# Performance work log

Hardware: AMD Instinct MI355X
Metric: run time of the kernel (lower is better)

The kernel has to match this reference:

```python
import jax, jax.numpy as jnp
import numpy as np

B, XDIM, S = 32768, 32, 16
N_COMBINE = XDIM - 2  # 30 combines with out_channels=S (block0 + middle blocks)


def setup_inputs() -> dict:
    key = jax.random.key(0)
    k1, k2, k3, k4 = jax.random.split(key, 4)
    x = jax.random.randint(k1, (B, XDIM), 0, 2, dtype=jnp.int32)  # binary data
    leaf_logits = jax.random.normal(k2, (XDIM, S), dtype=jnp.float32)  # Bernoulli leaf logits per var
    sum_weights = jax.random.normal(k3, (N_COMBINE, S * S, S), dtype=jnp.float32)
    sum_weights_last = jax.random.normal(k4, (S * S, 1), dtype=jnp.float32)
    return {"x": x, "leaf_logits": leaf_logits, "sum_weights": sum_weights,
            "sum_weights_last": sum_weights_last}


def _combine(a, b, W):
    # a, b: [B, S] log-likelihoods; W: [S*S, OC] raw sum weights.
    # CrossProduct in log domain: out[:, i*S + j] = a[:, i] + b[:, j]
    cross = (a[:, :, None] + b[:, None, :]).reshape(a.shape[0], S * S)  # [B, S*S]
    logw = jax.nn.log_softmax(W, axis=0)  # normalize over in_channels
    # Sum node in log domain: logsumexp over input channels
    return jax.nn.logsumexp(cross[:, :, None] + logw[None, :, :], axis=1)  # [B, OC]


def reference(x, leaf_logits, sum_weights, sum_weights_last):
    xf = x.astype(jnp.float32)[:, :, None]  # [B, XDIM, 1]
    # Bernoulli leaf log-prob: x*log(sigmoid(l)) + (1-x)*log(1-sigmoid(l))
    lp = (xf * jax.nn.log_sigmoid(leaf_logits)[None]
          + (1.0 - xf) * jax.nn.log_sigmoid(-leaf_logits)[None])  # [B, XDIM, S]

    # block 0: combine leaves of vars 0 and 1
    curr = _combine(lp[:, 0], lp[:, 1], sum_weights[0])  # [B, S]

    # middle blocks: fold in vars 2 .. XDIM-2
    mid_leaves = jnp.swapaxes(lp[:, 2:XDIM - 1], 0, 1)  # [XDIM-3, B, S]

    def step(c, inp):
        leaf, W = inp
        return _combine(c, leaf, W), None

    curr, _ = jax.lax.scan(step, curr, (mid_leaves, sum_weights[1:]))

    # final block: fold in last var with out_channels=1 root sum
    out = _combine(curr, lp[:, XDIM - 1], sum_weights_last)  # [B, 1]
    return out[:, None, :]  # [B, 1, 1] to match torch output shape
```

## Files before the change

kernel.cpp:

```cpp
#include <hip/hip_runtime.h>

using uint = unsigned int;

#define DW_LO    0
#define DW_HIb   7616
#define DW_FT    15232
#define DW_DELTA 15360
#define DW_BASE  15392
#define DW_EB0   15396
#define DW_TOT   15616

template<int K>
__device__ __forceinline__ int roti(int x) {
    return __builtin_amdgcn_update_dpp(0, x, 0x120 | K, 0xF, 0xF, true);
}
template<int K>
__device__ __forceinline__ float rotf(float x) {
    return __builtin_bit_cast(float, roti<K>(__builtin_bit_cast(int, x)));
}
__device__ __forceinline__ float logsig(float z) {
    return fminf(z, 0.f) - log1pf(__expf(-fabsf(z)));
}
__device__ __forceinline__ uint bfpack(float a, float b) {
    uint ua = __builtin_bit_cast(uint, a);
    uint ub = __builtin_bit_cast(uint, b);
    ua = (ua + 0x7fffu + ((ua >> 16) & 1u)) >> 16;
    ub = ((ub + 0x7fffu + ((ub >> 16) & 1u)) >> 16) << 16;
    return ua | ub;
}
__device__ __forceinline__ float blo(uint u) { return __builtin_bit_cast(float, u << 16); }
__device__ __forceinline__ float bhi(uint u) { return __builtin_bit_cast(float, u & 0xffff0000u); }

__global__ __launch_bounds__(1024) void prep(const float* __restrict__ sw,
                                             const float* __restrict__ swl,
                                             const float* __restrict__ ll,
                                             float* __restrict__ ws) {
    __shared__ __align__(16) float SW[16384];
    __shared__ float EB[128];
    __shared__ float CM[64], CS[64];
    __shared__ float WF[2048];
    __shared__ float T12[2048];
    __shared__ float MM[4096];
    __shared__ float WL[32];
    __shared__ float BMs[64];

    const int tid = threadIdx.x;
    const int t = blockIdx.x;
    const int lid = tid & 15;

    int s1 = roti<1>(lid) & 15,   s2 = roti<2>(lid) & 15,   s3 = roti<3>(lid) & 15;
    int s4 = roti<4>(lid) & 15,   s5 = roti<5>(lid) & 15,   s6 = roti<6>(lid) & 15;
    int s7 = roti<7>(lid) & 15,   s8 = roti<8>(lid) & 15,   s9 = roti<9>(lid) & 15;
    int s10 = roti<10>(lid) & 15, s11 = roti<11>(lid) & 15, s12 = roti<12>(lid) & 15;
    int s13 = roti<13>(lid) & 15, s14 = roti<14>(lid) & 15, s15 = roti<15>(lid) & 15;

    if (t < 7) {
        const float4* src = (const float4*)sw + t * 4096;
        #pragma unroll
        for (int k = 0; k < 4; ++k) ((float4*)SW)[tid + 1024 * k] = src[tid + 1024 * k];
        if (tid < 128) {
            int cc = tid >> 5, bb = (tid >> 4) & 1, var = 4 * t + 1 + cc;
            float l = ll[var * 16 + lid];
            float lp = bb ? logsig(l) : logsig(-l);
            float m = lp;
            m = fmaxf(m, rotf<1>(m)); m = fmaxf(m, rotf<2>(m));
            m = fmaxf(m, rotf<4>(m)); m = fmaxf(m, rotf<8>(m));
            EB[tid] = __expf(lp - m);
        }
        __syncthreads();
        {
            int grp = tid >> 4, cc = grp >> 4, ocx = grp & 15;
            float m = -1e30f;
            #pragma unroll
            for (int i = 0; i < 16; ++i)
                m = fmaxf(m, SW[cc * 4096 + i * 256 + lid * 16 + ocx]);
            m = fmaxf(m, rotf<1>(m)); m = fmaxf(m, rotf<2>(m));
            m = fmaxf(m, rotf<4>(m)); m = fmaxf(m, rotf<8>(m));
            if (lid == 0) CM[grp] = m;
        }
        __syncthreads();
        {
            int base = tid * 16;
            const float* cmp = CM + ((base >> 12) << 4);
            #pragma unroll
            for (int e = 0; e < 16; ++e) SW[base + e] = __expf(SW[base + e] - cmp[e]);
        }
        __syncthreads();
        {
            int grp = tid >> 4, cc = grp >> 4, ocx = grp & 15;
            float s = 0.f;
            #pragma unroll
            for (int i = 0; i < 16; ++i) s += SW[cc * 4096 + i * 256 + lid * 16 + ocx];
            s += rotf<1>(s); s += rotf<2>(s); s += rotf<4>(s); s += rotf<8>(s);
            if (lid == 0) CS[grp] = 1.0f / s;
        }
        __syncthreads();
        #pragma unroll
        for (int q = 0; q < 2; ++q) {
            int e = tid + q * 1024;
            int cb = e >> 8, cc = cb >> 1, i = (e >> 4) & 15, ocx = e & 15;
            float a = 0.f;
            #pragma unroll
            for (int j = 0; j < 16; ++j)
                a += EB[cb * 16 + j] * SW[cc * 4096 + i * 256 + j * 16 + ocx];
            WF[e] = a * CS[cc * 16 + ocx];
        }
        __syncthreads();
        {
            int bb = tid >> 8, i = (tid >> 4) & 15, l = lid;
            float a = 0.f, a2 = 0.f;
            #pragma unroll
            for (int k = 0; k < 16; ++k) {
                a  += WF[(bb & 1) * 256 + i * 16 + k]       * WF[(2 + (bb >> 1)) * 256 + k * 16 + l];
                a2 += WF[(4 + (bb & 1)) * 256 + i * 16 + k] * WF[(6 + (bb >> 1)) * 256 + k * 16 + l];
            }
            T12[tid] = a;
            T12[1024 + tid] = a2;
        }
        __syncthreads();
        #pragma unroll
        for (int q = 0; q < 4; ++q) {
            int e = tid + q * 1024;
            int v = e >> 8, i = (e >> 4) & 15, ocx = e & 15;
            float a = 0.f;
            #pragma unroll
            for (int k = 0; k < 16; ++k)
                a += T12[(v & 3) * 256 + i * 16 + k] * T12[1024 + (v >> 2) * 256 + k * 16 + ocx];
            MM[e] = a;
        }
        __syncthreads();
        if (tid < 256) {
            int v = tid >> 4, ocx = lid;
            const float* m = MM + v * 256;
            float x0 = m[ocx * 16 + ocx];
            float x1 = m[s1 * 16 + ocx],   x2 = m[s2 * 16 + ocx],   x3 = m[s3 * 16 + ocx];
            float x4 = m[s4 * 16 + ocx],   x5 = m[s5 * 16 + ocx],   x6 = m[s6 * 16 + ocx];
            float x7 = m[s7 * 16 + ocx],   x8 = m[s8 * 16 + ocx],   x9 = m[s9 * 16 + ocx];
            float x10 = m[s10 * 16 + ocx], x11 = m[s11 * 16 + ocx], x12 = m[s12 * 16 + ocx];
            float x13 = m[s13 * 16 + ocx], x14 = m[s14 * 16 + ocx], x15 = m[s15 * 16 + ocx];
            uint4 lo4, hi4;
            lo4.x = bfpack(x0, x1);   lo4.y = bfpack(x2, x3);
            lo4.z = bfpack(x4, x5);   lo4.w = bfpack(x6, x7);
            hi4.x = bfpack(x8, x9);   hi4.y = bfpack(x10, x11);
            hi4.z = bfpack(x12, x13); hi4.w = bfpack(x14, x15);
            uint* wsu = (uint*)ws;
            int dw = t * 1088 + v * 68 + ocx * 4;
            *(uint4*)(wsu + dw) = lo4;
            *(uint4*)(wsu + DW_HIb + dw) = hi4;
        }
    } else {
        const float4* s28 = (const float4*)(sw + 28 * 4096);
        #pragma unroll
        for (int k = 0; k < 2; ++k) ((float4*)SW)[tid + 1024 * k] = s28[tid + 1024 * k];
        if (tid < 64) ((float4*)SW)[2048 + tid] = ((const float4*)swl)[tid];
        if (tid < 96) {
            int cb = tid >> 4, bb = cb & 1;
            int var = (cb < 4) ? (29 + (cb >> 1)) : 31;
            float l = ll[var * 16 + lid];
            float lp = bb ? logsig(l) : logsig(-l);
            float m = lp;
            m = fmaxf(m, rotf<1>(m)); m = fmaxf(m, rotf<2>(m));
            m = fmaxf(m, rotf<4>(m)); m = fmaxf(m, rotf<8>(m));
            EB[tid] = __expf(lp - m);
        }
        __syncthreads();
        if (tid < 528) {
            int grp = tid >> 4;
            float m = -1e30f;
            if (grp < 32) {
                int cc = grp >> 4, ocx = grp & 15;
                #pragma unroll
                for (int i = 0; i < 16; ++i)
                    m = fmaxf(m, SW[cc * 4096 + i * 256 + lid * 16 + ocx]);
            } else {
                #pragma unroll
                for (int i = 0; i < 16; ++i)
                    m = fmaxf(m, SW[8192 + i * 16 + lid]);
            }
            m = fmaxf(m, rotf<1>(m)); m = fmaxf(m, rotf<2>(m));
            m = fmaxf(m, rotf<4>(m)); m = fmaxf(m, rotf<8>(m));
            if (lid == 0) CM[grp] = m;
        }
        __syncthreads();
        for (int idx = tid; idx < 8448; idx += 1024) {
            float cm = (idx < 8192) ? CM[((idx >> 12) << 4) | (idx & 15)] : CM[32];
            SW[idx] = __expf(SW[idx] - cm);
        }
        __syncthreads();
        if (tid < 528) {
            int grp = tid >> 4;
            float s = 0.f;
            if (grp < 32) {
                int cc = grp >> 4, ocx = grp & 15;
                #pragma unroll
                for (int i = 0; i < 16; ++i) s += SW[cc * 4096 + i * 256 + lid * 16 + ocx];
            } else {
                #pragma unroll
                for (int i = 0; i < 16; ++i) s += SW[8192 + i * 16 + lid];
            }
            s += rotf<1>(s); s += rotf<2>(s); s += rotf<4>(s); s += rotf<8>(s);
            if (lid == 0) CS[grp] = 1.0f / s;
        }
        __syncthreads();
        {
            int cb = tid >> 8, cc = cb >> 1, i = (tid >> 4) & 15, ocx = lid;
            float a = 0.f;
            #pragma unroll
            for (int j = 0; j < 16; ++j)
                a += EB[cb * 16 + j] * SW[cc * 4096 + i * 256 + j * 16 + ocx];
            WF[tid] = a * CS[cc * 16 + ocx];
        }
        if (tid < 32) {
            int bb = tid >> 4;
            float a = 0.f;
            #pragma unroll
            for (int j = 0; j < 16; ++j)
                a += EB[(4 + bb) * 16 + j] * SW[8192 + lid * 16 + j];
            WL[tid] = a * CS[32];
        }
        __syncthreads();
        {
            int b01 = tid >> 8, i = (tid >> 4) & 15, l = lid;
            float a = 0.f;
            #pragma unroll
            for (int k = 0; k < 16; ++k)
                a += WF[(b01 & 1) * 256 + i * 16 + k] * WF[(2 + (b01 >> 1)) * 256 + k * 16 + l];
            T12[tid] = a;
        }
        __syncthreads();
        if (tid < 128) {
            int v = tid >> 4;
            float a = 0.f;
            #pragma unroll
            for (int l = 0; l < 16; ++l)
                a += T12[(v & 3) * 256 + lid * 16 + l] * WL[(v >> 2) * 16 + l];
            ws[DW_FT + v * 16 + lid] = a;
        }
        if (tid >= 128 && tid < 192) {
            int u = tid - 128, var = u >> 1, bb = u & 1;
            float m = -1e30f;
            #pragma unroll
            for (int j = 0; j < 16; ++j) {
                float l = ll[var * 16 + j];
                m = fmaxf(m, bb ? logsig(l) : logsig(-l));
            }
            BMs[u] = m;
        }
        if (tid >= 192 && tid < 224) {
            int u = tid - 192, bb = u >> 4, j = u & 15;
            float m = -1e30f;
            #pragma unroll
            for (int jj = 0; jj < 16; ++jj) {
                float l = ll[jj];
                m = fmaxf(m, bb ? logsig(l) : logsig(-l));
            }
            float l = ll[j];
            ws[DW_EB0 + u] = __expf((bb ? logsig(l) : logsig(-l)) - m);
        }
        __syncthreads();
        if (tid < 32) ws[DW_DELTA + tid] = BMs[2 * tid + 1] - BMs[2 * tid];
        if (tid >= 64 && tid < 128) {
            int u = tid - 64;
            float vb = (u < 32) ? BMs[2 * u] : 0.f;
            #pragma unroll
            for (int off = 32; off >= 1; off >>= 1) vb += __shfl_xor(vb, off);
            if (u == 0) ws[DW_BASE] = vb;
        }
    }
}

__global__ __launch_bounds__(512, 4) void spn_main(const int* __restrict__ x,
                                                   const float* __restrict__ ws,
                                                   float* __restrict__ out) {
    __shared__ __align__(16) float sL[DW_TOT];
    const int tid = threadIdx.x;
    const int g = tid >> 4, oc = tid & 15;
    const int b = blockIdx.x * 32 + g;

    int2 xv = *(const int2*)(x + b * 32 + 2 * oc);
    unsigned long long m0 = __ballot(xv.x & 1);
    unsigned long long m1 = __ballot(xv.y & 1);
    const int gw = g & 3;
    unsigned be = (unsigned)(m0 >> (gw * 16)) & 0xffffu;
    unsigned bo = (unsigned)(m1 >> (gw * 16)) & 0xffffu;
    unsigned bits = 0;
    #pragma unroll
    for (int k = 0; k < 16; ++k)
        bits |= (((be >> k) & 1u) << (2 * k)) | (((bo >> k) & 1u) << (2 * k + 1));

    for (int k = tid; k < DW_TOT / 4; k += 512)
        ((float4*)sL)[k] = ((const float4*)ws)[k];
    __syncthreads();

    float2 dl = *(const float2*)(sL + DW_DELTA + 2 * oc);
    float part = 0.f;
    if (xv.x & 1) part += dl.x;
    if (xv.y & 1) part += dl.y;
    part += rotf<1>(part); part += rotf<2>(part);
    part += rotf<4>(part); part += rotf<8>(part);
    float L = sL[DW_BASE] + part;

    float acc = sL[DW_EB0 + (bits & 1) * 16 + oc];
    const uint* sPT = (const uint*)sL;
    const int ocd = oc * 4;

    #pragma unroll
    for (int p = 0; p < 7; ++p) {
        int v = (bits >> (4 * p + 1)) & 15;
        int dw = p * 1088 + v * 68 + ocd;
        uint4 wl4 = *(const uint4*)(sPT + dw);
        uint4 wh4 = *(const uint4*)(sPT + DW_HIb + dw);

        float a1 = rotf<1>(acc),   a2 = rotf<2>(acc),   a3 = rotf<3>(acc);
        float a4 = rotf<4>(acc),   a5 = rotf<5>(acc),   a6 = rotf<6>(acc);
        float a7 = rotf<7>(acc),   a8 = rotf<8>(acc),   a9 = rotf<9>(acc);
        float a10 = rotf<10>(acc), a11 = rotf<11>(acc), a12 = rotf<12>(acc);
        float a13 = rotf<13>(acc), a14 = rotf<14>(acc), a15 = rotf<15>(acc);

        float d0 = acc * blo(wl4.x);
        d0 = fmaf(a1, bhi(wl4.x), d0);
        d0 = fmaf(a2, blo(wl4.y), d0);
        d0 = fmaf(a3, bhi(wl4.y), d0);
        d0 = fmaf(a4, blo(wl4.z), d0);
        d0 = fmaf(a5, bhi(wl4.z), d0);
        d0 = fmaf(a6, blo(wl4.w), d0);
        d0 = fmaf(a7, bhi(wl4.w), d0);
        float d1 = a8 * blo(wh4.x);
        d1 = fmaf(a9,  bhi(wh4.x), d1);
        d1 = fmaf(a10, blo(wh4.y), d1);
        d1 = fmaf(a11, bhi(wh4.y), d1);
        d1 = fmaf(a12, blo(wh4.z), d1);
        d1 = fmaf(a13, bhi(wh4.z), d1);
        d1 = fmaf(a14, blo(wh4.w), d1);
        d1 = fmaf(a15, bhi(wh4.w), d1);
        float d = d0 + d1;

        if (p & 1) {
            float mm = fmaxf(d, rotf<1>(d));
            mm = fmaxf(mm, rotf<2>(mm));
            mm = fmaxf(mm, rotf<4>(mm));
            mm = fmaxf(mm, rotf<8>(mm));
            acc = d * __builtin_amdgcn_rcpf(mm);
            L += __logf(mm);
        } else {
            acc = d;
        }
    }

    int v3 = (bits >> 29) & 7;
    float ts = acc * sL[DW_FT + v3 * 16 + oc];
    ts += rotf<1>(ts); ts += rotf<2>(ts);
    ts += rotf<4>(ts); ts += rotf<8>(ts);
    if (oc == 0) out[b] = L + __logf(ts);
}

extern "C" void kernel_launch(void* const* d_in, const int* in_sizes, int n_in,
                              void* d_out, int out_size, void* d_ws, size_t ws_size,
                              hipStream_t stream) {
    const int*   x   = (const int*)d_in[0];
    const float* ll  = (const float*)d_in[1];
    const float* sw  = (const float*)d_in[2];
    const float* swl = (const float*)d_in[3];
    float* out = (float*)d_out;
    float* ws  = (float*)d_ws;

    hipLaunchKernelGGL(prep,     dim3(8),    dim3(1024), 0, stream, sw, swl, ll, ws);
    hipLaunchKernelGGL(spn_main, dim3(1024), dim3(512),  0, stream, x, ws, out);
}
```

Baseline: 25.76 us.

## Process two batch rows per thread group and restructure prep column reductions

The main kernel now has each 16-lane group handle two batch rows with independent accumulator chains. It launches half as many blocks, which halves the redundant per-block copy of the shared weight table into LDS and interleaves two dependent DPP/FMA chains for more instruction-level parallelism. The bit-interleave loop is replaced by a bit-spread trick. In prep, the strided per-column max/sum reductions become a two-stage partial reduction through a new shared PM buffer, which avoids strided LDS access. The cost is higher register pressure per thread and fewer blocks in flight.

```diff
diff --git a/kernel.cpp b/kernel.cpp
--- a/kernel.cpp
+++ b/kernel.cpp
@@ -18,6 +18,15 @@
 __device__ __forceinline__ float rotf(float x) {
     return __builtin_bit_cast(float, roti<K>(__builtin_bit_cast(int, x)));
 }
+__device__ __forceinline__ float rowmax16(float d) {
+    d = fmaxf(d, rotf<1>(d)); d = fmaxf(d, rotf<2>(d));
+    d = fmaxf(d, rotf<4>(d)); d = fmaxf(d, rotf<8>(d));
+    return d;
+}
+__device__ __forceinline__ float rowsum16(float d) {
+    d += rotf<1>(d); d += rotf<2>(d); d += rotf<4>(d); d += rotf<8>(d);
+    return d;
+}
 __device__ __forceinline__ float logsig(float z) {
     return fminf(z, 0.f) - log1pf(__expf(-fabsf(z)));
 }
@@ -30,14 +39,23 @@
 }
 __device__ __forceinline__ float blo(uint u) { return __builtin_bit_cast(float, u << 16); }
 __device__ __forceinline__ float bhi(uint u) { return __builtin_bit_cast(float, u & 0xffff0000u); }
+__device__ __forceinline__ unsigned spread16(unsigned u) {
+    u = (u | (u << 8)) & 0x00FF00FFu;
+    u = (u | (u << 4)) & 0x0F0F0F0Fu;
+    u = (u | (u << 2)) & 0x33333333u;
+    u = (u | (u << 1)) & 0x55555555u;
+    return u;
+}
 
 __global__ __launch_bounds__(1024) void prep(const float* __restrict__ sw,
                                              const float* __restrict__ swl,
                                              const float* __restrict__ ll,
                                              float* __restrict__ ws) {
     __shared__ __align__(16) float SW[16384];
+    __shared__ float PM[1024];
     __shared__ float EB[128];
     __shared__ float CM[64], CS[64];
+    __shared__ float CMl, CSl;
     __shared__ float WF[2048];
     __shared__ float T12[2048];
     __shared__ float MM[4096];
@@ -62,37 +80,48 @@
             int cc = tid >> 5, bb = (tid >> 4) & 1, var = 4 * t + 1 + cc;
             float l = ll[var * 16 + lid];
             float lp = bb ? logsig(l) : logsig(-l);
-            float m = lp;
-            m = fmaxf(m, rotf<1>(m)); m = fmaxf(m, rotf<2>(m));
-            m = fmaxf(m, rotf<4>(m)); m = fmaxf(m, rotf<8>(m));
-            EB[tid] = __expf(lp - m);
-        }
-        __syncthreads();
-        {
-            int grp = tid >> 4, cc = grp >> 4, ocx = grp & 15;
+            EB[tid] = __expf(lp - rowmax16(lp));
+        }
+        __syncthreads();
+        {
+            int grp = tid >> 4, cc = grp >> 4, r = grp & 15;
             float m = -1e30f;
             #pragma unroll
-            for (int i = 0; i < 16; ++i)
-                m = fmaxf(m, SW[cc * 4096 + i * 256 + lid * 16 + ocx]);
-            m = fmaxf(m, rotf<1>(m)); m = fmaxf(m, rotf<2>(m));
-            m = fmaxf(m, rotf<4>(m)); m = fmaxf(m, rotf<8>(m));
-            if (lid == 0) CM[grp] = m;
+            for (int q = 0; q < 16; ++q)
+                m = fmaxf(m, SW[cc * 4096 + (r * 16 + q) * 16 + lid]);
+            PM[grp * 16 + lid] = m;
+        }
+        __syncthreads();
+        if (tid < 64) {
+            int cc = tid >> 4, ocx = tid & 15;
+            float m = -1e30f;
+            #pragma unroll
+            for (int r = 0; r < 16; ++r) m = fmaxf(m, PM[(cc * 16 + r) * 16 + ocx]);
+            CM[tid] = m;
         }
         __syncthreads();
         {
             int base = tid * 16;
-            const float* cmp = CM + ((base >> 12) << 4);
+            const float* cmp = CM + ((tid >> 8) << 4);
             #pragma unroll
             for (int e = 0; e < 16; ++e) SW[base + e] = __expf(SW[base + e] - cmp[e]);
         }
         __syncthreads();
         {
-            int grp = tid >> 4, cc = grp >> 4, ocx = grp & 15;
+            int grp = tid >> 4, cc = grp >> 4, r = grp & 15;
             float s = 0.f;
             #pragma unroll
-            for (int i = 0; i < 16; ++i) s += SW[cc * 4096 + i * 256 + lid * 16 + ocx];
-            s += rotf<1>(s); s += rotf<2>(s); s += rotf<4>(s); s += rotf<8>(s);
-            if (lid == 0) CS[grp] = 1.0f / s;
+            for (int q = 0; q < 16; ++q)
+                s += SW[cc * 4096 + (r * 16 + q) * 16 + lid];
+            PM[grp * 16 + lid] = s;
+        }
+        __syncthreads();
+        if (tid < 64) {
+            int cc = tid >> 4, ocx = tid & 15;
+            float s = 0.f;
+            #pragma unroll
+            for (int r = 0; r < 16; ++r) s += PM[(cc * 16 + r) * 16 + ocx];
+            CS[tid] = 1.0f / s;
         }
         __syncthreads();
         #pragma unroll
@@ -158,48 +187,64 @@
             int var = (cb < 4) ? (29 + (cb >> 1)) : 31;
             float l = ll[var * 16 + lid];
             float lp = bb ? logsig(l) : logsig(-l);
-            float m = lp;
-            m = fmaxf(m, rotf<1>(m)); m = fmaxf(m, rotf<2>(m));
-            m = fmaxf(m, rotf<4>(m)); m = fmaxf(m, rotf<8>(m));
-            EB[tid] = __expf(lp - m);
-        }
-        __syncthreads();
-        if (tid < 528) {
+            EB[tid] = __expf(lp - rowmax16(lp));
+        }
+        __syncthreads();
+        {
             int grp = tid >> 4;
+            if (grp < 32) {
+                int cc = grp >> 4, r = grp & 15;
+                float m = -1e30f;
+                #pragma unroll
+                for (int q = 0; q < 16; ++q)
+                    m = fmaxf(m, SW[cc * 4096 + (r * 16 + q) * 16 + lid]);
+                PM[grp * 16 + lid] = m;
+            } else if (grp == 32) {
+                float m = -1e30f;
+                #pragma unroll
+                for (int q = 0; q < 16; ++q) m = fmaxf(m, SW[8192 + q * 16 + lid]);
+                m = rowmax16(m);
+                if (lid == 0) CMl = m;
+            }
+        }
+        __syncthreads();
+        if (tid < 32) {
+            int cc = tid >> 4, ocx = tid & 15;
             float m = -1e30f;
+            #pragma unroll
+            for (int r = 0; r < 16; ++r) m = fmaxf(m, PM[(cc * 16 + r) * 16 + ocx]);
+            CM[tid] = m;
+        }
+        __syncthreads();
+        for (int idx = tid; idx < 8448; idx += 1024) {
+            float cm = (idx < 8192) ? CM[((idx >> 12) << 4) | (idx & 15)] : CMl;
+            SW[idx] = __expf(SW[idx] - cm);
+        }
+        __syncthreads();
+        {
+            int grp = tid >> 4;
             if (grp < 32) {
-                int cc = grp >> 4, ocx = grp & 15;
+                int cc = grp >> 4, r = grp & 15;
+                float s = 0.f;
                 #pragma unroll
-                for (int i = 0; i < 16; ++i)
-                    m = fmaxf(m, SW[cc * 4096 + i * 256 + lid * 16 + ocx]);
-            } else {
+                for (int q = 0; q < 16; ++q)
+                    s += SW[cc * 4096 + (r * 16 + q) * 16 + lid];
+                PM[grp * 16 + lid] = s;
+            } else if (grp == 32) {
+                float s = 0.f;
                 #pragma unroll
-                for (int i = 0; i < 16; ++i)
-                    m = fmaxf(m, SW[8192 + i * 16 + lid]);
+                for (int q = 0; q < 16; ++q) s += SW[8192 + q * 16 + lid];
+                s = rowsum16(s);
+                if (lid == 0) CSl = 1.0f / s;
             }
-            m = fmaxf(m, rotf<1>(m)); m = fmaxf(m, rotf<2>(m));
-            m = fmaxf(m, rotf<4>(m)); m = fmaxf(m, rotf<8>(m));
-            if (lid == 0) CM[grp] = m;
-        }
-        __syncthreads();
-        for (int idx = tid; idx < 8448; idx += 1024) {
-            float cm = (idx < 8192) ? CM[((idx >> 12) << 4) | (idx & 15)] : CM[32];
-            SW[idx] = __expf(SW[idx] - cm);
-        }
-        __syncthreads();
-        if (tid < 528) {
-            int grp = tid >> 4;
+        }
+        __syncthreads();
+        if (tid < 32) {
+            int cc = tid >> 4, ocx = tid & 15;
             float s = 0.f;
-            if (grp < 32) {
-                int cc = grp >> 4, ocx = grp & 15;
-                #pragma unroll
-                for (int i = 0; i < 16; ++i) s += SW[cc * 4096 + i * 256 + lid * 16 + ocx];
-            } else {
-                #pragma unroll
-                for (int i = 0; i < 16; ++i) s += SW[8192 + i * 16 + lid];
-            }
-            s += rotf<1>(s); s += rotf<2>(s); s += rotf<4>(s); s += rotf<8>(s);
-            if (lid == 0) CS[grp] = 1.0f / s;
+            #pragma unroll
+            for (int r = 0; r < 16; ++r) s += PM[(cc * 16 + r) * 16 + ocx];
+            CS[tid] = 1.0f / s;
         }
         __syncthreads();
         {
@@ -216,7 +261,7 @@
             #pragma unroll
             for (int j = 0; j < 16; ++j)
                 a += EB[(4 + bb) * 16 + j] * SW[8192 + lid * 16 + j];
-            WL[tid] = a * CS[32];
+            WL[tid] = a * CSl;
         }
         __syncthreads();
         {
@@ -269,89 +314,88 @@
     }
 }
 
+__device__ __forceinline__ float quadstep(const uint* sPT, float acc, int dw) {
+    uint4 wl4 = *(const uint4*)(sPT + dw);
+    uint4 wh4 = *(const uint4*)(sPT + DW_HIb + dw);
+    float d0 = acc * blo(wl4.x);
+    d0 = fmaf(rotf<1>(acc), bhi(wl4.x), d0);
+    d0 = fmaf(rotf<2>(acc), blo(wl4.y), d0);
+    d0 = fmaf(rotf<3>(acc), bhi(wl4.y), d0);
+    d0 = fmaf(rotf<4>(acc), blo(wl4.z), d0);
+    d0 = fmaf(rotf<5>(acc), bhi(wl4.z), d0);
+    d0 = fmaf(rotf<6>(acc), blo(wl4.w), d0);
+    d0 = fmaf(rotf<7>(acc), bhi(wl4.w), d0);
+    float d1 = rotf<8>(acc) * blo(wh4.x);
+    d1 = fmaf(rotf<9>(acc),  bhi(wh4.x), d1);
+    d1 = fmaf(rotf<10>(acc), blo(wh4.y), d1);
+    d1 = fmaf(rotf<11>(acc), bhi(wh4.y), d1);
+    d1 = fmaf(rotf<12>(acc), blo(wh4.z), d1);
+    d1 = fmaf(rotf<13>(acc), bhi(wh4.z), d1);
+    d1 = fmaf(rotf<14>(acc), blo(wh4.w), d1);
+    d1 = fmaf(rotf<15>(acc), bhi(wh4.w), d1);
+    return d0 + d1;
+}
+
 __global__ __launch_bounds__(512, 4) void spn_main(const int* __restrict__ x,
                                                    const float* __restrict__ ws,
                                                    float* __restrict__ out) {
     __shared__ __align__(16) float sL[DW_TOT];
     const int tid = threadIdx.x;
     const int g = tid >> 4, oc = tid & 15;
-    const int b = blockIdx.x * 32 + g;
-
-    int2 xv = *(const int2*)(x + b * 32 + 2 * oc);
-    unsigned long long m0 = __ballot(xv.x & 1);
-    unsigned long long m1 = __ballot(xv.y & 1);
+    const int b0 = blockIdx.x * 64 + g;
+    const int b1 = b0 + 32;
+
+    int2 xa = *(const int2*)(x + b0 * 32 + 2 * oc);
+    int2 xb = *(const int2*)(x + b1 * 32 + 2 * oc);
+    unsigned long long ma0 = __ballot(xa.x & 1);
+    unsigned long long ma1 = __ballot(xa.y & 1);
+    unsigned long long mb0 = __ballot(xb.x & 1);
+    unsigned long long mb1 = __ballot(xb.y & 1);
     const int gw = g & 3;
-    unsigned be = (unsigned)(m0 >> (gw * 16)) & 0xffffu;
-    unsigned bo = (unsigned)(m1 >> (gw * 16)) & 0xffffu;
-    unsigned bits = 0;
-    #pragma unroll
-    for (int k = 0; k < 16; ++k)
-        bits |= (((be >> k) & 1u) << (2 * k)) | (((bo >> k) & 1u) << (2 * k + 1));
+    unsigned bitsA = spread16((unsigned)(ma0 >> (gw * 16)) & 0xffffu)
+                   | (spread16((unsigned)(ma1 >> (gw * 16)) & 0xffffu) << 1);
+    unsigned bitsB = spread16((unsigned)(mb0 >> (gw * 16)) & 0xffffu)
+                   | (spread16((unsigned)(mb1 >> (gw * 16)) & 0xffffu) << 1);
 
     for (int k = tid; k < DW_TOT / 4; k += 512)
         ((float4*)sL)[k] = ((const float4*)ws)[k];
     __syncthreads();
 
     float2 dl = *(const float2*)(sL + DW_DELTA + 2 * oc);
-    float part = 0.f;
-    if (xv.x & 1) part += dl.x;
-    if (xv.y & 1) part += dl.y;
-    part += rotf<1>(part); part += rotf<2>(part);
-    part += rotf<4>(part); part += rotf<8>(part);
-    float L = sL[DW_BASE] + part;
-
-    float acc = sL[DW_EB0 + (bits & 1) * 16 + oc];
+    float pa = ((xa.x & 1) ? dl.x : 0.f) + ((xa.y & 1) ? dl.y : 0.f);
+    float pb = ((xb.x & 1) ? dl.x : 0.f) + ((xb.y & 1) ? dl.y : 0.f);
+    float base = sL[DW_BASE];
+    float LA = base + rowsum16(pa);
+    float LB = base + rowsum16(pb);
+
+    float accA = sL[DW_EB0 + (bitsA & 1) * 16 + oc];
+    float accB = sL[DW_EB0 + (bitsB & 1) * 16 + oc];
     const uint* sPT = (const uint*)sL;
     const int ocd = oc * 4;
 
     #pragma unroll
     for (int p = 0; p < 7; ++p) {
-        int v = (bits >> (4 * p + 1)) & 15;
-        int dw = p * 1088 + v * 68 + ocd;
-        uint4 wl4 = *(const uint4*)(sPT + dw);
-        uint4 wh4 = *(const uint4*)(sPT + DW_HIb + dw);
-
-        float a1 = rotf<1>(acc),   a2 = rotf<2>(acc),   a3 = rotf<3>(acc);
-        float a4 = rotf<4>(acc),   a5 = rotf<5>(acc),   a6 = rotf<6>(acc);
-        float a7 = rotf<7>(acc),   a8 = rotf<8>(acc),   a9 = rotf<9>(acc);
-        float a10 = rotf<10>(acc), a11 = rotf<11>(acc), a12 = rotf<12>(acc);
-        float a13 = rotf<13>(acc), a14 = rotf<14>(acc), a15 = rotf<15>(acc);
-
-        float d0 = acc * blo(wl4.x);
-        d0 = fmaf(a1, bhi(wl4.x), d0);
-        d0 = fmaf(a2, blo(wl4.y), d0);
-        d0 = fmaf(a3, bhi(wl4.y), d0);
-        d0 = fmaf(a4, blo(wl4.z), d0);
-        d0 = fmaf(a5, bhi(wl4.z), d0);
-        d0 = fmaf(a6, blo(wl4.w), d0);
-        d0 = fmaf(a7, bhi(wl4.w), d0);
-        float d1 = a8 * blo(wh4.x);
-        d1 = fmaf(a9,  bhi(wh4.x), d1);
-        d1 = fmaf(a10, blo(wh4.y), d1);
-        d1 = fmaf(a11, bhi(wh4.y), d1);
-        d1 = fmaf(a12, blo(wh4.z), d1);
-        d1 = fmaf(a13, bhi(wh4.z), d1);
-        d1 = fmaf(a14, blo(wh4.w), d1);
-        d1 = fmaf(a15, bhi(wh4.w), d1);
-        float d = d0 + d1;
-
+        int dwA = p * 1088 + (int)((bitsA >> (4 * p + 1)) & 15) * 68 + ocd;
+        int dwB = p * 1088 + (int)((bitsB >> (4 * p + 1)) & 15) * 68 + ocd;
+        float dA = quadstep(sPT, accA, dwA);
+        float dB = quadstep(sPT, accB, dwB);
         if (p & 1) {
-            float mm = fmaxf(d, rotf<1>(d));
-            mm = fmaxf(mm, rotf<2>(mm));
-            mm = fmaxf(mm, rotf<4>(mm));
-            mm = fmaxf(mm, rotf<8>(mm));
-            acc = d * __builtin_amdgcn_rcpf(mm);
-            L += __logf(mm);
+            float mA = rowmax16(dA), mB = rowmax16(dB);
+            accA = dA * __builtin_amdgcn_rcpf(mA);
+            accB = dB * __builtin_amdgcn_rcpf(mB);
+            LA += __logf(mA);
+            LB += __logf(mB);
         } else {
-            acc = d;
+            accA = dA; accB = dB;
         }
     }
 
-    int v3 = (bits >> 29) & 7;
-    float ts = acc * sL[DW_FT + v3 * 16 + oc];
-    ts += rotf<1>(ts); ts += rotf<2>(ts);
-    ts += rotf<4>(ts); ts += rotf<8>(ts);
-    if (oc == 0) out[b] = L + __logf(ts);
+    float tsA = rowsum16(accA * sL[DW_FT + ((bitsA >> 29) & 7) * 16 + oc]);
+    float tsB = rowsum16(accB * sL[DW_FT + ((bitsB >> 29) & 7) * 16 + oc]);
+    if (oc == 0) {
+        out[b0] = LA + __logf(tsA);
+        out[b1] = LB + __logf(tsB);
+    }
 }
 
 extern "C" void kernel_launch(void* const* d_in, const int* in_sizes, int n_in,
@@ -364,6 +408,6 @@
     float* out = (float*)d_out;
     float* ws  = (float*)d_ws;
 
-    hipLaunchKernelGGL(prep,     dim3(8),    dim3(1024), 0, stream, sw, swl, ll, ws);
-    hipLaunchKernelGGL(spn_main, dim3(1024), dim3(512),  0, stream, x, ws, out);
-}
+    hipLaunchKernelGGL(prep,     dim3(8),   dim3(1024), 0, stream, sw, swl, ll, ws);
+    hipLaunchKernelGGL(spn_main, dim3(512), dim3(512),  0, stream, x, ws, out);
+}
```

New measurement: 23.49 us. 1.1x faster.
